# Kernel optimization log

Hardware: AMD Instinct MI355X
Metric: run time of the kernel (lower is better)

The kernel has to match this reference:

```python
import jax, jax.numpy as jnp
import numpy as np

KERN = 2  # matches init kwarg


def _avgpool(x):
    # non-overlapping avg pool kernel=stride=KERN on (N,C,H,W)
    N, C, H, W = x.shape
    return x.reshape(N, C, H // KERN, KERN, W // KERN, KERN).mean(axis=(3, 5))


def _pair_sum(mu1, var1, mu2, var2):
    # mu*, var*: (N, D). Broadcast to (N, N, D) and reduce to scalar.
    d = mu1[:, None, :] - mu2[None, :, :]
    s = var1[:, None, :] + var2[None, :, :]
    return jnp.sum(jnp.exp(-0.5 * (d * d / s + jnp.log(s))))


def setup_inputs() -> dict:
    key = jax.random.key(0)
    k1, k2, k3, k4 = jax.random.split(key, 4)
    shp = (128, 16, 32, 32)
    return {
        "mu_a": jax.random.normal(k1, shp, dtype=jnp.float32),
        "logvar_a": jax.random.normal(k2, shp, dtype=jnp.float32),
        "mu_b": jax.random.normal(k3, shp, dtype=jnp.float32),
        "logvar_b": jax.random.normal(k4, shp, dtype=jnp.float32),
    }


def reference(mu_a, logvar_a, mu_b, logvar_b):
    inv_k2 = 1.0 / (KERN * KERN)
    ma = _avgpool(mu_a)
    mb = _avgpool(mu_b)
    va = _avgpool(jnp.exp(logvar_a)) * inv_k2
    vb = _avgpool(jnp.exp(logvar_b)) * inv_k2
    N = ma.shape[0]
    ma, mb = ma.reshape(N, -1), mb.reshape(N, -1)
    va, vb = va.reshape(N, -1), vb.reshape(N, -1)
    vaa = _pair_sum(ma, va, ma, va)
    vab = _pair_sum(ma, va, mb, vb)
    vbb = _pair_sum(mb, vb, mb, vb)
    return vaa + vbb - 2.0 * vab
```

## Files before the change

### kernel.cpp

```cpp
#include <hip/hip_runtime.h>

#define NN 128
#define CC_ 16
#define HH 32
#define WW 32
#define DD 4096
#define ND (NN*DD)

typedef float v2f __attribute__((ext_vector_type(2)));

#define MU_SCALE 0.8493218002880191f

__global__ __launch_bounds__(256) void pool_kernel(
    const float* __restrict__ mu_a, const float* __restrict__ lv_a,
    const float* __restrict__ mu_b, const float* __restrict__ lv_b,
    float4* __restrict__ wmv, float* __restrict__ out)
{
    int t = blockIdx.x * 256 + threadIdx.x;
    if (t == 0) out[0] = 0.0f;

    int wo = t & 15;
    int ho = (t >> 4) & 15;
    int c  = (t >> 8) & 15;
    int n  = t >> 12;

    int base = ((n * CC_ + c) * HH + 2 * ho) * WW + 2 * wo;

    float2 a0 = *(const float2*)(mu_a + base);
    float2 a1 = *(const float2*)(mu_a + base + WW);
    float2 la0 = *(const float2*)(lv_a + base);
    float2 la1 = *(const float2*)(lv_a + base + WW);
    float2 b0 = *(const float2*)(mu_b + base);
    float2 b1 = *(const float2*)(mu_b + base + WW);
    float2 lb0 = *(const float2*)(lv_b + base);
    float2 lb1 = *(const float2*)(lv_b + base + WW);

    const float ms = 0.25f * MU_SCALE;
    float ma_v = ms * (a0.x + a0.y + a1.x + a1.y);
    float mb_v = ms * (b0.x + b0.y + b1.x + b1.y);
    float va_v = 0.0625f * (__expf(la0.x) + __expf(la0.y) + __expf(la1.x) + __expf(la1.y));
    float vb_v = 0.0625f * (__expf(lb0.x) + __expf(lb0.y) + __expf(lb1.x) + __expf(lb1.y));

    wmv[t] = make_float4(ma_v, mb_v, va_v, vb_v);
}

__device__ __forceinline__ void pair_group(
    v2f& acc, v2f mi, v2f mj, v2f vi, v2f vj)
{
    v2f dd = mi - mj;
    v2f s  = vi + vj;
    v2f r;
    r.x = __builtin_amdgcn_rsqf(s.x);
    r.y = __builtin_amdgcn_rsqf(s.y);
    v2f q  = dd * r;
    v2f qq = q * q;
    v2f e;
    e.x = __builtin_amdgcn_exp2f(-qq.x);
    e.y = __builtin_amdgcn_exp2f(-qq.y);
    acc += e * r;
}

__device__ __forceinline__ void pair_group_w(
    v2f& acc, v2f w, v2f mi, v2f mj, v2f vi, v2f vj)
{
    v2f dd = mi - mj;
    v2f s  = vi + vj;
    v2f r;
    r.x = __builtin_amdgcn_rsqf(s.x);
    r.y = __builtin_amdgcn_rsqf(s.y);
    v2f q  = dd * r;
    v2f qq = q * q;
    v2f e;
    e.x = __builtin_amdgcn_exp2f(-qq.x);
    e.y = __builtin_amdgcn_exp2f(-qq.y);
    v2f er = e * r;
    acc += w * er;
}

__device__ __forceinline__ void run_range(
    int jlo, int jhi, int i0, int d,
    const float4* __restrict__ wmv,
    v2f& acc_aa, v2f& acc_bb, v2f& acc_ab,
    const v2f pma[2], const v2f pmb[2], const v2f pva[2], const v2f pvb[2])
{
    const int below_end = min(jhi, i0);
    const int band_lo   = max(jlo, i0);
    const int band_hi   = min(jhi, i0 + 4);
    const int above_lo  = max(jlo, i0 + 4);

#pragma unroll 2
    for (int j = jlo; j < below_end; ++j) {
        float4 jr = wmv[j * DD + d];
        v2f jma2 = (v2f){jr.x, jr.x};
        v2f jmb2 = (v2f){jr.y, jr.y};
        v2f jva2 = (v2f){jr.z, jr.z};
        v2f jvb2 = (v2f){jr.w, jr.w};
#pragma unroll
        for (int p = 0; p < 2; ++p) {
            pair_group(acc_aa, pma[p], jma2, pva[p], jva2);
            pair_group(acc_bb, pmb[p], jmb2, pvb[p], jvb2);
            pair_group(acc_ab, pma[p], jmb2, pva[p], jvb2);
        }
    }

    for (int j = band_lo; j < band_hi; ++j) {
        float4 jr = wmv[j * DD + d];
        v2f jma2 = (v2f){jr.x, jr.x};
        v2f jmb2 = (v2f){jr.y, jr.y};
        v2f jva2 = (v2f){jr.z, jr.z};
        v2f jvb2 = (v2f){jr.w, jr.w};
        v2f w[2];
#pragma unroll
        for (int p = 0; p < 2; ++p) {
            int r0 = i0 + 2 * p, r1 = r0 + 1;
            w[p].x = (j < r0) ? 1.0f : (j == r0 ? 0.5f : 0.0f);
            w[p].y = (j < r1) ? 1.0f : (j == r1 ? 0.5f : 0.0f);
        }
#pragma unroll
        for (int p = 0; p < 2; ++p) {
            pair_group_w(acc_aa, w[p], pma[p], jma2, pva[p], jva2);
            pair_group_w(acc_bb, w[p], pmb[p], jmb2, pvb[p], jvb2);
            pair_group(acc_ab, pma[p], jmb2, pva[p], jvb2);
        }
    }

#pragma unroll 2
    for (int j = above_lo; j < jhi; ++j) {
        float4 jr = wmv[j * DD + d];
        v2f jmb2 = (v2f){jr.y, jr.y};
        v2f jvb2 = (v2f){jr.w, jr.w};
#pragma unroll
        for (int p = 0; p < 2; ++p) {
            pair_group(acc_ab, pma[p], jmb2, pva[p], jvb2);
        }
    }
}

__device__ __forceinline__ void process_unit(
    int tile, int chunk, int d, const float4* __restrict__ wmv,
    v2f& acc_aa, v2f& acc_bb, v2f& acc_ab)
{
    const int i0 = tile * 4;
    v2f pma[2], pmb[2], pva[2], pvb[2];
#pragma unroll
    for (int p = 0; p < 2; ++p) {
        float4 r0 = wmv[(i0 + 2 * p) * DD + d];
        float4 r1 = wmv[(i0 + 2 * p + 1) * DD + d];
        pma[p] = (v2f){r0.x, r1.x};
        pmb[p] = (v2f){r0.y, r1.y};
        pva[p] = (v2f){r0.z, r1.z};
        pvb[p] = (v2f){r0.w, r1.w};
    }
    run_range(chunk * 16, chunk * 16 + 16, i0, d, wmv,
              acc_aa, acc_bb, acc_ab, pma, pmb, pva, pvb);
}

__device__ __forceinline__ uint2 heavy_below(int k) {
    int tile, c;
    if (k < 16)      { tile = 16 + (k >> 2);            c = k & 3; }
    else if (k < 36) { int kk = k - 16; tile = 20 + kk / 5; c = kk % 5; }
    else if (k < 60) { int kk = k - 36; tile = 24 + kk / 6; c = kk % 6; }
    else             { int kk = k - 60; tile = 28 + kk / 7; c = kk % 7; }
    return make_uint2(tile, c);
}
__device__ __forceinline__ uint2 light_above(int k) {
    int tile, c;
    if (k < 28)      { tile = k / 7;                    c = 1 + k % 7; }
    else if (k < 52) { int kk = k - 28; tile = 4 + kk / 6;  c = 2 + kk % 6; }
    else if (k < 72) { int kk = k - 52; tile = 8 + kk / 5;  c = 3 + kk % 5; }
    else             { int kk = k - 72; tile = 12 + (kk >> 2); c = 4 + (kk & 3); }
    return make_uint2(tile, c);
}
__device__ __forceinline__ uint2 light_below(int k) {
    int tile, c;
    if (k < 4)       { tile = 4 + k;                    c = 0; }
    else if (k < 12) { int kk = k - 4;  tile = 8 + (kk >> 1);  c = kk & 1; }
    else             { int kk = k - 12; tile = 12 + kk / 3; c = kk % 3; }
    return make_uint2(tile, c);
}
__device__ __forceinline__ uint2 heavy_above(int k) {
    int tile, c;
    if (k < 12)      { tile = 16 + k / 3;               c = 5 + k % 3; }
    else if (k < 20) { int kk = k - 12; tile = 20 + (kk >> 1); c = 6 + (kk & 1); }
    else             { tile = 24 + (k - 20);            c = 7; }
    return make_uint2(tile, c);
}

__global__ __launch_bounds__(256) void pair_kernel(
    const float4* __restrict__ wmv, float* __restrict__ out)
{
    const int d = blockIdx.x * 256 + threadIdx.x;
    const int y = blockIdx.y;

    uint2 A, B;
    if (y < 88)       { A = heavy_below(y);       B = light_above(y); }
    else if (y < 112) { A = light_below(y - 88);  B = heavy_above(y - 88); }
    else              { int k = y - 112;
                        A = make_uint2(k, k >> 2);
                        B = make_uint2(31 - k, (31 - k) >> 2); }

    v2f acc_aa = (v2f){0.0f, 0.0f};
    v2f acc_bb = (v2f){0.0f, 0.0f};
    v2f acc_ab = (v2f){0.0f, 0.0f};

    process_unit((int)A.x, (int)A.y, d, wmv, acc_aa, acc_bb, acc_ab);
    process_unit((int)B.x, (int)B.y, d, wmv, acc_aa, acc_bb, acc_ab);

    float part = 2.0f * ((acc_aa.x + acc_aa.y) + (acc_bb.x + acc_bb.y)
                       - (acc_ab.x + acc_ab.y));

#pragma unroll
    for (int off = 32; off > 0; off >>= 1)
        part += __shfl_down(part, off, 64);

    __shared__ float wsum[4];
    int lane = threadIdx.x & 63;
    int wv_  = threadIdx.x >> 6;
    if (lane == 0) wsum[wv_] = part;
    __syncthreads();
    if (threadIdx.x == 0) {
        float s = wsum[0] + wsum[1] + wsum[2] + wsum[3];
        atomicAdd(out, s);
    }
}

extern "C" void kernel_launch(void* const* d_in, const int* in_sizes, int n_in,
                              void* d_out, int out_size, void* d_ws, size_t ws_size,
                              hipStream_t stream) {
    const float* mu_a = (const float*)d_in[0];
    const float* lv_a = (const float*)d_in[1];
    const float* mu_b = (const float*)d_in[2];
    const float* lv_b = (const float*)d_in[3];
    float* out  = (float*)d_out;
    float4* wmv = (float4*)d_ws;

    pool_kernel<<<dim3(ND / 256), 256, 0, stream>>>(mu_a, lv_a, mu_b, lv_b, wmv, out);
    pair_kernel<<<dim3(DD / 256, 128), 256, 0, stream>>>(wmv, out);
}
```

Measured before the change: 113.7 us.

## Split paired work units into separate blocks and add dual accumulators for ILP

Each block of the pair kernel now processes a single (tile, chunk) unit instead of two balanced units, so the grid's y dimension doubles from 128 to 256 blocks. The inner j loops are manually unrolled by two with independent accumulator sets, which breaks the serial dependency chains on the accumulators and lets the two rows' loads issue together. The goal is more parallelism, both across blocks and within each thread. The cost is that per-block work is no longer balanced (heavy and light units were previously paired), and there are twice as many atomic adds and block reductions.

```diff
diff --git a/kernel.cpp b/kernel.cpp
--- a/kernel.cpp
+++ b/kernel.cpp
@@ -77,6 +77,33 @@
     acc += w * er;
 }
 
+__device__ __forceinline__ void do_full(
+    float4 jr, v2f& aa, v2f& bb, v2f& ab,
+    const v2f pma[2], const v2f pmb[2], const v2f pva[2], const v2f pvb[2])
+{
+    v2f jma2 = (v2f){jr.x, jr.x};
+    v2f jmb2 = (v2f){jr.y, jr.y};
+    v2f jva2 = (v2f){jr.z, jr.z};
+    v2f jvb2 = (v2f){jr.w, jr.w};
+#pragma unroll
+    for (int p = 0; p < 2; ++p) {
+        pair_group(aa, pma[p], jma2, pva[p], jva2);
+        pair_group(bb, pmb[p], jmb2, pvb[p], jvb2);
+        pair_group(ab, pma[p], jmb2, pva[p], jvb2);
+    }
+}
+
+__device__ __forceinline__ void do_ab(
+    float4 jr, v2f& ab, const v2f pma[2], const v2f pva[2])
+{
+    v2f jmb2 = (v2f){jr.y, jr.y};
+    v2f jvb2 = (v2f){jr.w, jr.w};
+#pragma unroll
+    for (int p = 0; p < 2; ++p) {
+        pair_group(ab, pma[p], jmb2, pva[p], jvb2);
+    }
+}
+
 __device__ __forceinline__ void run_range(
     int jlo, int jhi, int i0, int d,
     const float4* __restrict__ wmv,
@@ -88,18 +115,22 @@
     const int band_hi   = min(jhi, i0 + 4);
     const int above_lo  = max(jlo, i0 + 4);
 
-#pragma unroll 2
-    for (int j = jlo; j < below_end; ++j) {
-        float4 jr = wmv[j * DD + d];
-        v2f jma2 = (v2f){jr.x, jr.x};
-        v2f jmb2 = (v2f){jr.y, jr.y};
-        v2f jva2 = (v2f){jr.z, jr.z};
-        v2f jvb2 = (v2f){jr.w, jr.w};
-#pragma unroll
-        for (int p = 0; p < 2; ++p) {
-            pair_group(acc_aa, pma[p], jma2, pva[p], jva2);
-            pair_group(acc_bb, pmb[p], jmb2, pvb[p], jvb2);
-            pair_group(acc_ab, pma[p], jmb2, pva[p], jvb2);
+    v2f aa2 = (v2f){0.0f, 0.0f};
+    v2f bb2 = (v2f){0.0f, 0.0f};
+    v2f ab2 = (v2f){0.0f, 0.0f};
+
+    {
+        int j = jlo;
+#pragma unroll 1
+        for (; j + 1 < below_end; j += 2) {
+            float4 jr0 = wmv[j * DD + d];
+            float4 jr1 = wmv[(j + 1) * DD + d];
+            do_full(jr0, acc_aa, acc_bb, acc_ab, pma, pmb, pva, pvb);
+            do_full(jr1, aa2, bb2, ab2, pma, pmb, pva, pvb);
+        }
+        if (j < below_end) {
+            float4 jr = wmv[j * DD + d];
+            do_full(jr, acc_aa, acc_bb, acc_ab, pma, pmb, pva, pvb);
         }
     }
 
@@ -124,16 +155,24 @@
         }
     }
 
-#pragma unroll 2
-    for (int j = above_lo; j < jhi; ++j) {
-        float4 jr = wmv[j * DD + d];
-        v2f jmb2 = (v2f){jr.y, jr.y};
-        v2f jvb2 = (v2f){jr.w, jr.w};
-#pragma unroll
-        for (int p = 0; p < 2; ++p) {
-            pair_group(acc_ab, pma[p], jmb2, pva[p], jvb2);
-        }
-    }
+    {
+        int j = above_lo;
+#pragma unroll 1
+        for (; j + 1 < jhi; j += 2) {
+            float4 jr0 = wmv[j * DD + d];
+            float4 jr1 = wmv[(j + 1) * DD + d];
+            do_ab(jr0, acc_ab, pma, pva);
+            do_ab(jr1, ab2, pma, pva);
+        }
+        if (j < jhi) {
+            float4 jr = wmv[j * DD + d];
+            do_ab(jr, acc_ab, pma, pva);
+        }
+    }
+
+    acc_aa += aa2;
+    acc_bb += bb2;
+    acc_ab += ab2;
 }
 
 __device__ __forceinline__ void process_unit(
@@ -190,21 +229,25 @@
     const float4* __restrict__ wmv, float* __restrict__ out)
 {
     const int d = blockIdx.x * 256 + threadIdx.x;
-    const int y = blockIdx.y;
-
-    uint2 A, B;
-    if (y < 88)       { A = heavy_below(y);       B = light_above(y); }
-    else if (y < 112) { A = light_below(y - 88);  B = heavy_above(y - 88); }
-    else              { int k = y - 112;
-                        A = make_uint2(k, k >> 2);
-                        B = make_uint2(31 - k, (31 - k) >> 2); }
+    const int yy = blockIdx.y;
+
+    uint2 U;
+    if (yy < 128) {
+        if (yy < 88)       U = heavy_below(yy);
+        else if (yy < 112) U = light_below(yy - 88);
+        else               { int k = yy - 112; U = make_uint2(k, k >> 2); }
+    } else {
+        int z = yy - 128;
+        if (z < 88)        U = light_above(z);
+        else if (z < 112)  U = heavy_above(z - 88);
+        else               { int k = z - 112; int t = 31 - k; U = make_uint2(t, t >> 2); }
+    }
 
     v2f acc_aa = (v2f){0.0f, 0.0f};
     v2f acc_bb = (v2f){0.0f, 0.0f};
     v2f acc_ab = (v2f){0.0f, 0.0f};
 
-    process_unit((int)A.x, (int)A.y, d, wmv, acc_aa, acc_bb, acc_ab);
-    process_unit((int)B.x, (int)B.y, d, wmv, acc_aa, acc_bb, acc_ab);
+    process_unit((int)U.x, (int)U.y, d, wmv, acc_aa, acc_bb, acc_ab);
 
     float part = 2.0f * ((acc_aa.x + acc_aa.y) + (acc_bb.x + acc_bb.y)
                        - (acc_ab.x + acc_ab.y));
@@ -235,5 +278,5 @@
     float4* wmv = (float4*)d_ws;
 
     pool_kernel<<<dim3(ND / 256), 256, 0, stream>>>(mu_a, lv_a, mu_b, lv_b, wmv, out);
-    pair_kernel<<<dim3(DD / 256, 128), 256, 0, stream>>>(wmv, out);
-}
+    pair_kernel<<<dim3(DD / 256, 256), 256, 0, stream>>>(wmv, out);
+}
```

Measured after the change: 138.3 us. 1.22x slower.

## Use 8-row i-tiles with one unit per block in pair kernel

Applied to the files above, without the earlier changes.

Each block now processes a single work unit covering an 8-row i-tile against a 16-column j-chunk, instead of two 4-row units. This is meant to double reuse of each loaded j row across more i rows and cut global loads per pair evaluation. A new unit_for mapping over 128 y-blocks replaces the heavy/light pairing used for load balancing. The cost is more registers per thread, and per-block work may be less even now that units are no longer paired.

```diff
diff --git a/kernel.cpp b/kernel.cpp
--- a/kernel.cpp
+++ b/kernel.cpp
@@ -77,16 +77,16 @@
     acc += w * er;
 }
 
-__device__ __forceinline__ void run_range(
+__device__ __forceinline__ void run_range8(
     int jlo, int jhi, int i0, int d,
     const float4* __restrict__ wmv,
     v2f& acc_aa, v2f& acc_bb, v2f& acc_ab,
-    const v2f pma[2], const v2f pmb[2], const v2f pva[2], const v2f pvb[2])
+    const v2f pma[4], const v2f pmb[4], const v2f pva[4], const v2f pvb[4])
 {
     const int below_end = min(jhi, i0);
     const int band_lo   = max(jlo, i0);
-    const int band_hi   = min(jhi, i0 + 4);
-    const int above_lo  = max(jlo, i0 + 4);
+    const int band_hi   = min(jhi, i0 + 8);
+    const int above_lo  = max(jlo, i0 + 8);
 
 #pragma unroll 2
     for (int j = jlo; j < below_end; ++j) {
@@ -96,7 +96,7 @@
         v2f jva2 = (v2f){jr.z, jr.z};
         v2f jvb2 = (v2f){jr.w, jr.w};
 #pragma unroll
-        for (int p = 0; p < 2; ++p) {
+        for (int p = 0; p < 4; ++p) {
             pair_group(acc_aa, pma[p], jma2, pva[p], jva2);
             pair_group(acc_bb, pmb[p], jmb2, pvb[p], jvb2);
             pair_group(acc_ab, pma[p], jmb2, pva[p], jvb2);
@@ -109,15 +109,15 @@
         v2f jmb2 = (v2f){jr.y, jr.y};
         v2f jva2 = (v2f){jr.z, jr.z};
         v2f jvb2 = (v2f){jr.w, jr.w};
-        v2f w[2];
-#pragma unroll
-        for (int p = 0; p < 2; ++p) {
+        v2f w[4];
+#pragma unroll
+        for (int p = 0; p < 4; ++p) {
             int r0 = i0 + 2 * p, r1 = r0 + 1;
             w[p].x = (j < r0) ? 1.0f : (j == r0 ? 0.5f : 0.0f);
             w[p].y = (j < r1) ? 1.0f : (j == r1 ? 0.5f : 0.0f);
         }
 #pragma unroll
-        for (int p = 0; p < 2; ++p) {
+        for (int p = 0; p < 4; ++p) {
             pair_group_w(acc_aa, w[p], pma[p], jma2, pva[p], jva2);
             pair_group_w(acc_bb, w[p], pmb[p], jmb2, pvb[p], jvb2);
             pair_group(acc_ab, pma[p], jmb2, pva[p], jvb2);
@@ -130,20 +130,20 @@
         v2f jmb2 = (v2f){jr.y, jr.y};
         v2f jvb2 = (v2f){jr.w, jr.w};
 #pragma unroll
-        for (int p = 0; p < 2; ++p) {
+        for (int p = 0; p < 4; ++p) {
             pair_group(acc_ab, pma[p], jmb2, pva[p], jvb2);
         }
     }
 }
 
-__device__ __forceinline__ void process_unit(
+__device__ __forceinline__ void process_unit8(
     int tile, int chunk, int d, const float4* __restrict__ wmv,
     v2f& acc_aa, v2f& acc_bb, v2f& acc_ab)
 {
-    const int i0 = tile * 4;
-    v2f pma[2], pmb[2], pva[2], pvb[2];
-#pragma unroll
-    for (int p = 0; p < 2; ++p) {
+    const int i0 = tile * 8;
+    v2f pma[4], pmb[4], pva[4], pvb[4];
+#pragma unroll
+    for (int p = 0; p < 4; ++p) {
         float4 r0 = wmv[(i0 + 2 * p) * DD + d];
         float4 r1 = wmv[(i0 + 2 * p + 1) * DD + d];
         pma[p] = (v2f){r0.x, r1.x};
@@ -151,60 +151,54 @@
         pva[p] = (v2f){r0.z, r1.z};
         pvb[p] = (v2f){r0.w, r1.w};
     }
-    run_range(chunk * 16, chunk * 16 + 16, i0, d, wmv,
-              acc_aa, acc_bb, acc_ab, pma, pmb, pva, pvb);
-}
-
-__device__ __forceinline__ uint2 heavy_below(int k) {
-    int tile, c;
-    if (k < 16)      { tile = 16 + (k >> 2);            c = k & 3; }
-    else if (k < 36) { int kk = k - 16; tile = 20 + kk / 5; c = kk % 5; }
-    else if (k < 60) { int kk = k - 36; tile = 24 + kk / 6; c = kk % 6; }
-    else             { int kk = k - 60; tile = 28 + kk / 7; c = kk % 7; }
-    return make_uint2(tile, c);
-}
-__device__ __forceinline__ uint2 light_above(int k) {
-    int tile, c;
-    if (k < 28)      { tile = k / 7;                    c = 1 + k % 7; }
-    else if (k < 52) { int kk = k - 28; tile = 4 + kk / 6;  c = 2 + kk % 6; }
-    else if (k < 72) { int kk = k - 52; tile = 8 + kk / 5;  c = 3 + kk % 5; }
-    else             { int kk = k - 72; tile = 12 + (kk >> 2); c = 4 + (kk & 3); }
-    return make_uint2(tile, c);
-}
-__device__ __forceinline__ uint2 light_below(int k) {
-    int tile, c;
-    if (k < 4)       { tile = 4 + k;                    c = 0; }
-    else if (k < 12) { int kk = k - 4;  tile = 8 + (kk >> 1);  c = kk & 1; }
-    else             { int kk = k - 12; tile = 12 + kk / 3; c = kk % 3; }
-    return make_uint2(tile, c);
-}
-__device__ __forceinline__ uint2 heavy_above(int k) {
-    int tile, c;
-    if (k < 12)      { tile = 16 + k / 3;               c = 5 + k % 3; }
-    else if (k < 20) { int kk = k - 12; tile = 20 + (kk >> 1); c = 6 + (kk & 1); }
-    else             { tile = 24 + (k - 20);            c = 7; }
-    return make_uint2(tile, c);
+    run_range8(chunk * 16, chunk * 16 + 16, i0, d, wmv,
+               acc_aa, acc_bb, acc_ab, pma, pmb, pva, pvb);
+}
+
+__device__ __forceinline__ uint2 unit_for(int y) {
+    if (y < 56) {
+        int u, kk;
+        if      (y < 2)  { u = 1; kk = y; }
+        else if (y < 6)  { u = 2; kk = y - 2; }
+        else if (y < 12) { u = 3; kk = y - 6; }
+        else if (y < 20) { u = 4; kk = y - 12; }
+        else if (y < 30) { u = 5; kk = y - 20; }
+        else if (y < 42) { u = 6; kk = y - 30; }
+        else             { u = 7; kk = y - 42; }
+        return make_uint2(2 * u + kk / u, kk % u);
+    } else if (y < 64) {
+        int u = y - 56;
+        return make_uint2(2 * u + 1, u);
+    } else if (y < 72) {
+        int u = y - 64;
+        return make_uint2(2 * u, u);
+    } else {
+        int k = y - 72;
+        int u, kk;
+        if      (k < 14) { u = 0; kk = k; }
+        else if (k < 26) { u = 1; kk = k - 14; }
+        else if (k < 36) { u = 2; kk = k - 26; }
+        else if (k < 44) { u = 3; kk = k - 36; }
+        else if (k < 50) { u = 4; kk = k - 44; }
+        else if (k < 54) { u = 5; kk = k - 50; }
+        else             { u = 6; kk = k - 54; }
+        int w = 7 - u;
+        return make_uint2(2 * u + kk / w, u + 1 + kk % w);
+    }
 }
 
 __global__ __launch_bounds__(256) void pair_kernel(
     const float4* __restrict__ wmv, float* __restrict__ out)
 {
     const int d = blockIdx.x * 256 + threadIdx.x;
-    const int y = blockIdx.y;
-
-    uint2 A, B;
-    if (y < 88)       { A = heavy_below(y);       B = light_above(y); }
-    else if (y < 112) { A = light_below(y - 88);  B = heavy_above(y - 88); }
-    else              { int k = y - 112;
-                        A = make_uint2(k, k >> 2);
-                        B = make_uint2(31 - k, (31 - k) >> 2); }
+
+    uint2 U = unit_for(blockIdx.y);
 
     v2f acc_aa = (v2f){0.0f, 0.0f};
     v2f acc_bb = (v2f){0.0f, 0.0f};
     v2f acc_ab = (v2f){0.0f, 0.0f};
 
-    process_unit((int)A.x, (int)A.y, d, wmv, acc_aa, acc_bb, acc_ab);
-    process_unit((int)B.x, (int)B.y, d, wmv, acc_aa, acc_bb, acc_ab);
+    process_unit8((int)U.x, (int)U.y, d, wmv, acc_aa, acc_bb, acc_ab);
 
     float part = 2.0f * ((acc_aa.x + acc_aa.y) + (acc_bb.x + acc_bb.y)
                        - (acc_ab.x + acc_ab.y));
```

Result: slower. 119.3 us (+4.9%).

## Split paired work units into one unit per block and batch transcendentals

Applied to the files above, without the earlier changes.

Each block now processes a single (tile, chunk) unit instead of two balanced units, and the grid y dimension doubles from 128 to 256. A new unit_for mapping enumerates below-diagonal, diagonal and above-diagonal units. Inner loops are restructured so all six rsq and exp operations per j are issued together, and the ab-only loop is unrolled 4. This is meant to raise parallelism and ILP, but block workloads are now uneven, which may cause tail imbalance, and more atomics are issued.

```diff
diff --git a/kernel.cpp b/kernel.cpp
--- a/kernel.cpp
+++ b/kernel.cpp
@@ -42,22 +42,6 @@
     float vb_v = 0.0625f * (__expf(lb0.x) + __expf(lb0.y) + __expf(lb1.x) + __expf(lb1.y));
 
     wmv[t] = make_float4(ma_v, mb_v, va_v, vb_v);
-}
-
-__device__ __forceinline__ void pair_group(
-    v2f& acc, v2f mi, v2f mj, v2f vi, v2f vj)
-{
-    v2f dd = mi - mj;
-    v2f s  = vi + vj;
-    v2f r;
-    r.x = __builtin_amdgcn_rsqf(s.x);
-    r.y = __builtin_amdgcn_rsqf(s.y);
-    v2f q  = dd * r;
-    v2f qq = q * q;
-    v2f e;
-    e.x = __builtin_amdgcn_exp2f(-qq.x);
-    e.y = __builtin_amdgcn_exp2f(-qq.y);
-    acc += e * r;
 }
 
 __device__ __forceinline__ void pair_group_w(
@@ -77,7 +61,95 @@
     acc += w * er;
 }
 
-__device__ __forceinline__ void run_range(
+__device__ __forceinline__ void pair_group(
+    v2f& acc, v2f mi, v2f mj, v2f vi, v2f vj)
+{
+    v2f dd = mi - mj;
+    v2f s  = vi + vj;
+    v2f r;
+    r.x = __builtin_amdgcn_rsqf(s.x);
+    r.y = __builtin_amdgcn_rsqf(s.y);
+    v2f q  = dd * r;
+    v2f qq = q * q;
+    v2f e;
+    e.x = __builtin_amdgcn_exp2f(-qq.x);
+    e.y = __builtin_amdgcn_exp2f(-qq.y);
+    acc += e * r;
+}
+
+__device__ __forceinline__ void do_full_phase(
+    float4 jr, v2f& aa, v2f& bb, v2f& ab,
+    const v2f pma[2], const v2f pmb[2], const v2f pva[2], const v2f pvb[2])
+{
+    v2f jma2 = (v2f){jr.x, jr.x};
+    v2f jmb2 = (v2f){jr.y, jr.y};
+    v2f jva2 = (v2f){jr.z, jr.z};
+    v2f jvb2 = (v2f){jr.w, jr.w};
+
+    v2f s[6], dd[6];
+    s[0] = pva[0] + jva2;  dd[0] = pma[0] - jma2;
+    s[1] = pva[1] + jva2;  dd[1] = pma[1] - jma2;
+    s[2] = pvb[0] + jvb2;  dd[2] = pmb[0] - jmb2;
+    s[3] = pvb[1] + jvb2;  dd[3] = pmb[1] - jmb2;
+    s[4] = pva[0] + jvb2;  dd[4] = pma[0] - jmb2;
+    s[5] = pva[1] + jvb2;  dd[5] = pma[1] - jmb2;
+
+    v2f r[6];
+#pragma unroll
+    for (int k = 0; k < 6; ++k) {
+        r[k].x = __builtin_amdgcn_rsqf(s[k].x);
+        r[k].y = __builtin_amdgcn_rsqf(s[k].y);
+    }
+    v2f qq[6];
+#pragma unroll
+    for (int k = 0; k < 6; ++k) {
+        v2f q = dd[k] * r[k];
+        qq[k] = q * q;
+    }
+    v2f e[6];
+#pragma unroll
+    for (int k = 0; k < 6; ++k) {
+        e[k].x = __builtin_amdgcn_exp2f(-qq[k].x);
+        e[k].y = __builtin_amdgcn_exp2f(-qq[k].y);
+    }
+    aa += e[0] * r[0];  aa += e[1] * r[1];
+    bb += e[2] * r[2];  bb += e[3] * r[3];
+    ab += e[4] * r[4];  ab += e[5] * r[5];
+}
+
+__device__ __forceinline__ void do_ab_phase(
+    float4 jr, v2f& ab, const v2f pma[2], const v2f pva[2])
+{
+    v2f jmb2 = (v2f){jr.y, jr.y};
+    v2f jvb2 = (v2f){jr.w, jr.w};
+
+    v2f s[2], dd[2];
+    s[0] = pva[0] + jvb2;  dd[0] = pma[0] - jmb2;
+    s[1] = pva[1] + jvb2;  dd[1] = pma[1] - jmb2;
+
+    v2f r[2];
+#pragma unroll
+    for (int k = 0; k < 2; ++k) {
+        r[k].x = __builtin_amdgcn_rsqf(s[k].x);
+        r[k].y = __builtin_amdgcn_rsqf(s[k].y);
+    }
+    v2f qq[2];
+#pragma unroll
+    for (int k = 0; k < 2; ++k) {
+        v2f q = dd[k] * r[k];
+        qq[k] = q * q;
+    }
+    v2f e[2];
+#pragma unroll
+    for (int k = 0; k < 2; ++k) {
+        e[k].x = __builtin_amdgcn_exp2f(-qq[k].x);
+        e[k].y = __builtin_amdgcn_exp2f(-qq[k].y);
+    }
+    ab += e[0] * r[0];
+    ab += e[1] * r[1];
+}
+
+__device__ __forceinline__ void run_range4(
     int jlo, int jhi, int i0, int d,
     const float4* __restrict__ wmv,
     v2f& acc_aa, v2f& acc_bb, v2f& acc_ab,
@@ -91,16 +163,7 @@
 #pragma unroll 2
     for (int j = jlo; j < below_end; ++j) {
         float4 jr = wmv[j * DD + d];
-        v2f jma2 = (v2f){jr.x, jr.x};
-        v2f jmb2 = (v2f){jr.y, jr.y};
-        v2f jva2 = (v2f){jr.z, jr.z};
-        v2f jvb2 = (v2f){jr.w, jr.w};
-#pragma unroll
-        for (int p = 0; p < 2; ++p) {
-            pair_group(acc_aa, pma[p], jma2, pva[p], jva2);
-            pair_group(acc_bb, pmb[p], jmb2, pvb[p], jvb2);
-            pair_group(acc_ab, pma[p], jmb2, pva[p], jvb2);
-        }
+        do_full_phase(jr, acc_aa, acc_bb, acc_ab, pma, pmb, pva, pvb);
     }
 
     for (int j = band_lo; j < band_hi; ++j) {
@@ -124,19 +187,14 @@
         }
     }
 
-#pragma unroll 2
+#pragma unroll 4
     for (int j = above_lo; j < jhi; ++j) {
         float4 jr = wmv[j * DD + d];
-        v2f jmb2 = (v2f){jr.y, jr.y};
-        v2f jvb2 = (v2f){jr.w, jr.w};
-#pragma unroll
-        for (int p = 0; p < 2; ++p) {
-            pair_group(acc_ab, pma[p], jmb2, pva[p], jvb2);
-        }
-    }
-}
-
-__device__ __forceinline__ void process_unit(
+        do_ab_phase(jr, acc_ab, pma, pva);
+    }
+}
+
+__device__ __forceinline__ void process_unit4(
     int tile, int chunk, int d, const float4* __restrict__ wmv,
     v2f& acc_aa, v2f& acc_bb, v2f& acc_ab)
 {
@@ -151,60 +209,51 @@
         pva[p] = (v2f){r0.z, r1.z};
         pvb[p] = (v2f){r0.w, r1.w};
     }
-    run_range(chunk * 16, chunk * 16 + 16, i0, d, wmv,
-              acc_aa, acc_bb, acc_ab, pma, pmb, pva, pvb);
-}
-
-__device__ __forceinline__ uint2 heavy_below(int k) {
-    int tile, c;
-    if (k < 16)      { tile = 16 + (k >> 2);            c = k & 3; }
-    else if (k < 36) { int kk = k - 16; tile = 20 + kk / 5; c = kk % 5; }
-    else if (k < 60) { int kk = k - 36; tile = 24 + kk / 6; c = kk % 6; }
-    else             { int kk = k - 60; tile = 28 + kk / 7; c = kk % 7; }
-    return make_uint2(tile, c);
-}
-__device__ __forceinline__ uint2 light_above(int k) {
-    int tile, c;
-    if (k < 28)      { tile = k / 7;                    c = 1 + k % 7; }
-    else if (k < 52) { int kk = k - 28; tile = 4 + kk / 6;  c = 2 + kk % 6; }
-    else if (k < 72) { int kk = k - 52; tile = 8 + kk / 5;  c = 3 + kk % 5; }
-    else             { int kk = k - 72; tile = 12 + (kk >> 2); c = 4 + (kk & 3); }
-    return make_uint2(tile, c);
-}
-__device__ __forceinline__ uint2 light_below(int k) {
-    int tile, c;
-    if (k < 4)       { tile = 4 + k;                    c = 0; }
-    else if (k < 12) { int kk = k - 4;  tile = 8 + (kk >> 1);  c = kk & 1; }
-    else             { int kk = k - 12; tile = 12 + kk / 3; c = kk % 3; }
-    return make_uint2(tile, c);
-}
-__device__ __forceinline__ uint2 heavy_above(int k) {
-    int tile, c;
-    if (k < 12)      { tile = 16 + k / 3;               c = 5 + k % 3; }
-    else if (k < 20) { int kk = k - 12; tile = 20 + (kk >> 1); c = 6 + (kk & 1); }
-    else             { tile = 24 + (k - 20);            c = 7; }
-    return make_uint2(tile, c);
+    run_range4(chunk * 16, chunk * 16 + 16, i0, d, wmv,
+               acc_aa, acc_bb, acc_ab, pma, pmb, pva, pvb);
+}
+
+__device__ __forceinline__ uint2 unit_for(int y) {
+    if (y < 112) {
+        int u, kk;
+        if      (y < 4)   { u = 1; kk = y; }
+        else if (y < 12)  { u = 2; kk = y - 4; }
+        else if (y < 24)  { u = 3; kk = y - 12; }
+        else if (y < 40)  { u = 4; kk = y - 24; }
+        else if (y < 60)  { u = 5; kk = y - 40; }
+        else if (y < 84)  { u = 6; kk = y - 60; }
+        else              { u = 7; kk = y - 84; }
+        return make_uint2(4 * u + kk / u, kk % u);
+    } else if (y < 144) {
+        int t = y - 112;
+        return make_uint2(t, t >> 2);
+    } else {
+        int k = y - 144;
+        int u, kk;
+        if      (k < 28)  { u = 0; kk = k; }
+        else if (k < 52)  { u = 1; kk = k - 28; }
+        else if (k < 72)  { u = 2; kk = k - 52; }
+        else if (k < 88)  { u = 3; kk = k - 72; }
+        else if (k < 100) { u = 4; kk = k - 88; }
+        else if (k < 108) { u = 5; kk = k - 100; }
+        else              { u = 6; kk = k - 108; }
+        int w = 7 - u;
+        return make_uint2(4 * u + kk / w, u + 1 + kk % w);
+    }
 }
 
 __global__ __launch_bounds__(256) void pair_kernel(
     const float4* __restrict__ wmv, float* __restrict__ out)
 {
     const int d = blockIdx.x * 256 + threadIdx.x;
-    const int y = blockIdx.y;
-
-    uint2 A, B;
-    if (y < 88)       { A = heavy_below(y);       B = light_above(y); }
-    else if (y < 112) { A = light_below(y - 88);  B = heavy_above(y - 88); }
-    else              { int k = y - 112;
-                        A = make_uint2(k, k >> 2);
-                        B = make_uint2(31 - k, (31 - k) >> 2); }
+
+    uint2 U = unit_for(blockIdx.y);
 
     v2f acc_aa = (v2f){0.0f, 0.0f};
     v2f acc_bb = (v2f){0.0f, 0.0f};
     v2f acc_ab = (v2f){0.0f, 0.0f};
 
-    process_unit((int)A.x, (int)A.y, d, wmv, acc_aa, acc_bb, acc_ab);
-    process_unit((int)B.x, (int)B.y, d, wmv, acc_aa, acc_bb, acc_ab);
+    process_unit4((int)U.x, (int)U.y, d, wmv, acc_aa, acc_bb, acc_ab);
 
     float part = 2.0f * ((acc_aa.x + acc_aa.y) + (acc_bb.x + acc_bb.y)
                        - (acc_ab.x + acc_ab.y));
@@ -235,5 +284,5 @@
     float4* wmv = (float4*)d_ws;
 
     pool_kernel<<<dim3(ND / 256), 256, 0, stream>>>(mu_a, lv_a, mu_b, lv_b, wmv, out);
-    pair_kernel<<<dim3(DD / 256, 128), 256, 0, stream>>>(wmv, out);
-}
+    pair_kernel<<<dim3(DD / 256, 256), 256, 0, stream>>>(wmv, out);
+}
```

Result: slower. 138.2 us (+21.5%).
